# Performance work log

Hardware: AMD Instinct MI355X
Metric: run time of the kernel (lower is better)

Reference implementation:

```python
import jax, jax.numpy as jnp
import numpy as np

N, E, F, H, C = 100000, 1600000, 32, 64, 10


def setup_inputs() -> dict:
    key = jax.random.key(0)
    ks = jax.random.split(key, 12)
    x = jax.random.normal(ks[0], (N, F), dtype=jnp.float32)
    edge_index = jax.random.randint(ks[1], (2, E), 0, N, dtype=jnp.int64)
    edge_attr = jax.random.uniform(ks[2], (E,), dtype=jnp.float32)
    s = lambda k, shp, fan: jax.random.normal(k, shp, dtype=jnp.float32) / np.sqrt(fan)
    return {
        "x": x,
        "edge_index": edge_index,
        "edge_attr": edge_attr,
        "W1_rel": s(ks[3], (H, F), F),
        "b1_rel": jnp.zeros((H,), jnp.float32),
        "W1_root": s(ks[4], (H, F), F),
        "W2_rel": s(ks[5], (H, H), H),
        "b2_rel": jnp.zeros((H,), jnp.float32),
        "W2_root": s(ks[6], (H, H), H),
        "fc_w": s(ks[7], (C, H), H),
        "fc_b": jnp.zeros((C,), jnp.float32),
    }


def graph_conv(x, src, dst, ew, W_rel, b_rel, W_root):
    # message: x_j * e_ji, scatter-add at destination nodes (PyG GraphConv, aggr='add')
    msg = x[src] * ew[:, None]            # [E, d] gather + scale
    agg = jax.ops.segment_sum(msg, dst, num_segments=N)  # [N, d]
    return agg @ W_rel.T + b_rel + x @ W_root.T


def reference(x, edge_index, edge_attr, W1_rel, b1_rel, W1_root, W2_rel, b2_rel, W2_root, fc_w, fc_b):
    src, dst = edge_index[0], edge_index[1]
    h = jax.nn.relu(graph_conv(x, src, dst, edge_attr, W1_rel, b1_rel, W1_root))
    h = jax.nn.relu(graph_conv(h, src, dst, edge_attr, W2_rel, b2_rel, W2_root))
    return h @ fc_w.T + fc_b
```

## Files before the change

### kernel.cpp

```cpp
#include <hip/hip_runtime.h>

#define N_NODES 100000
#define EDGES   1600000
#define SCAN_NB ((N_NODES + 511) / 512)
#define GRID_HEAVY 2048

__device__ __forceinline__ unsigned pack_bf16(float a, float b) {
    unsigned ua = (__float_as_uint(a) + 0x8000u) >> 16;
    unsigned ub = (__float_as_uint(b) + 0x8000u) & 0xffff0000u;
    return ub | ua;
}
__device__ __forceinline__ float bflo(unsigned p) { return __uint_as_float(p << 16); }
__device__ __forceinline__ float bfhi(unsigned p) { return __uint_as_float(p & 0xffff0000u); }
__device__ __forceinline__ float bf2f(unsigned short u) { return __uint_as_float(((unsigned)u) << 16); }
__device__ __forceinline__ unsigned short f2bf(float x) { return (unsigned short)((__float_as_uint(x) + 0x8000u) >> 16); }

#define WAVE_FENCE() asm volatile("s_waitcnt lgkmcnt(0)" ::: "memory")

__global__ __launch_bounds__(256) void prep_kernel(
    const float* __restrict__ x, const int* __restrict__ ei,
    unsigned short* __restrict__ xb, int* __restrict__ cnt)
{
    int t = blockIdx.x * 256 + threadIdx.x;
    if (t < N_NODES * 32) xb[t] = f2bf(x[t]);
    if (t < EDGES) atomicAdd(&cnt[ei[EDGES + t]], 1);
}

__global__ __launch_bounds__(512) void scan1_kernel(
    const int* __restrict__ cnt, int* __restrict__ part, int* __restrict__ bsum)
{
    __shared__ int s[512];
    int tid = threadIdx.x;
    int gid = blockIdx.x * 512 + tid;
    int v = (gid < N_NODES) ? cnt[gid] : 0;
    s[tid] = v;
    __syncthreads();
    for (int off = 1; off < 512; off <<= 1) {
        int t = (tid >= off) ? s[tid - off] : 0;
        __syncthreads();
        s[tid] += t;
        __syncthreads();
    }
    if (gid < N_NODES) part[gid] = s[tid] - v;
    if (tid == 511) bsum[blockIdx.x] = s[511];
}

__global__ __launch_bounds__(256) void scan2_kernel(
    const int* __restrict__ bsum, int* __restrict__ bsumx)
{
    __shared__ int s[256];
    int tid = threadIdx.x;
    int v = (tid < SCAN_NB) ? bsum[tid] : 0;
    s[tid] = v;
    __syncthreads();
    for (int off = 1; off < 256; off <<= 1) {
        int t = (tid >= off) ? s[tid - off] : 0;
        __syncthreads();
        s[tid] += t;
        __syncthreads();
    }
    bsumx[tid] = s[tid] - v;
}

__global__ __launch_bounds__(512) void scan3_kernel(
    const int* __restrict__ part, const int* __restrict__ bsumx,
    int* __restrict__ offs, int* __restrict__ cursor)
{
    int gid = blockIdx.x * 512 + threadIdx.x;
    if (gid < N_NODES) {
        int o = part[gid] + bsumx[blockIdx.x];
        offs[gid] = o;
        cursor[gid] = o;
    }
    if (gid == 0) offs[N_NODES] = EDGES;
}

__global__ __launch_bounds__(256) void fill_kernel(
    const int* __restrict__ ei, const float* __restrict__ ew,
    int* __restrict__ cursor, uint2* __restrict__ bucket)
{
    int e = blockIdx.x * 256 + threadIdx.x;
    if (e >= EDGES) return;
    int d = ei[EDGES + e];
    int pos = atomicAdd(&cursor[d], 1);
    uint2 slot;
    slot.x = (unsigned)ei[e];
    slot.y = __float_as_uint(ew[e]);
    bucket[pos] = slot;
}

__global__ __launch_bounds__(256, 6) void agg_dense1_kernel(
    const float* __restrict__ x, const unsigned short* __restrict__ xb,
    const uint2* __restrict__ bucket, const int* __restrict__ offs,
    const float* __restrict__ W_rel, const float* __restrict__ b_rel,
    const float* __restrict__ W_root, unsigned short* __restrict__ h1b)
{
    __shared__ unsigned pkrel[16][64];
    __shared__ unsigned pkroot[16][64];
    __shared__ float sb[64];
    __shared__ __align__(16) float accr[4][32];
    __shared__ __align__(16) float xr[4][32];
    int tid = threadIdx.x;
    for (int i = tid; i < 16 * 64; i += 256) {
        int k = i >> 6, h = i & 63;
        pkrel[k][h]  = pack_bf16(W_rel[h * 32 + 2 * k],  W_rel[h * 32 + 2 * k + 1]);
        pkroot[k][h] = pack_bf16(W_root[h * 32 + 2 * k], W_root[h * 32 + 2 * k + 1]);
    }
    if (tid < 64) sb[tid] = b_rel[tid];
    __syncthreads();

    int w = tid >> 6, lane = tid & 63;
    int sub = lane >> 5, f = lane & 31;
    int wid = blockIdx.x * 4 + w;

    for (int node = wid; node < N_NODES; node += GRID_HEAVY * 4) {
        float acc = 0.f;
        if (sub == 0) xr[w][f] = x[(size_t)node * 32 + f];
        int o0 = __builtin_amdgcn_readfirstlane(offs[node]);
        int o1 = __builtin_amdgcn_readfirstlane(offs[node + 1]);
        int j = o0;
        for (; j + 8 <= o1; j += 8) {
            uint2 b0 = bucket[j + 0 + sub], b1 = bucket[j + 2 + sub];
            uint2 b2 = bucket[j + 4 + sub], b3 = bucket[j + 6 + sub];
            float v0 = bf2f(xb[(size_t)b0.x * 32 + f]);
            float v1 = bf2f(xb[(size_t)b1.x * 32 + f]);
            float v2 = bf2f(xb[(size_t)b2.x * 32 + f]);
            float v3 = bf2f(xb[(size_t)b3.x * 32 + f]);
            acc += v0 * __uint_as_float(b0.y) + v1 * __uint_as_float(b1.y)
                 + v2 * __uint_as_float(b2.y) + v3 * __uint_as_float(b3.y);
        }
        for (; j + 2 <= o1; j += 2) {
            uint2 b = bucket[j + sub];
            acc += bf2f(xb[(size_t)b.x * 32 + f]) * __uint_as_float(b.y);
        }
        if (j + sub < o1) {
            uint2 b = bucket[j + sub];
            acc += bf2f(xb[(size_t)b.x * 32 + f]) * __uint_as_float(b.y);
        }
        acc += __shfl_xor(acc, 32);
        if (sub == 0) accr[w][f] = acc;
        WAVE_FENCE();
        {
            const float2* ap = (const float2*)accr[w];
            const float2* xp = (const float2*)xr[w];
            float sum = sb[lane];
            #pragma unroll
            for (int k = 0; k < 16; ++k) {
                float2 a = ap[k], xv = xp[k];
                unsigned pr = pkrel[k][lane], po = pkroot[k][lane];
                sum += a.x * bflo(pr) + a.y * bfhi(pr)
                     + xv.x * bflo(po) + xv.y * bfhi(po);
            }
            h1b[(size_t)node * 64 + lane] = f2bf(fmaxf(sum, 0.f));
        }
        WAVE_FENCE();
    }
}

__global__ __launch_bounds__(256, 6) void agg_dense2_kernel(
    const unsigned short* __restrict__ h1b, const uint2* __restrict__ bucket,
    const int* __restrict__ offs,
    const float* __restrict__ W_rel, const float* __restrict__ b_rel,
    const float* __restrict__ W_root,
    const float* __restrict__ fc_w, const float* __restrict__ fc_b,
    float* __restrict__ out)
{
    __shared__ unsigned pkrel[32][64];
    __shared__ unsigned pkroot[32][64];
    __shared__ unsigned pkfc[32][10];
    __shared__ float sb[64], sfb[10];
    __shared__ __align__(16) float accr[4][64];
    __shared__ __align__(16) float hvr[4][64];
    __shared__ __align__(16) float sh2r[4][64];
    int tid = threadIdx.x;
    for (int i = tid; i < 32 * 64; i += 256) {
        int k = i >> 6, h = i & 63;
        pkrel[k][h]  = pack_bf16(W_rel[h * 64 + 2 * k],  W_rel[h * 64 + 2 * k + 1]);
        pkroot[k][h] = pack_bf16(W_root[h * 64 + 2 * k], W_root[h * 64 + 2 * k + 1]);
    }
    for (int i = tid; i < 32 * 10; i += 256) {
        int k = i % 32, c = i / 32;
        pkfc[k][c] = pack_bf16(fc_w[c * 64 + 2 * k], fc_w[c * 64 + 2 * k + 1]);
    }
    if (tid < 64) sb[tid] = b_rel[tid];
    if (tid < 10) sfb[tid] = fc_b[tid];
    __syncthreads();

    int w = tid >> 6, lane = tid & 63;
    int wid = blockIdx.x * 4 + w;

    for (int node = wid; node < N_NODES; node += GRID_HEAVY * 4) {
        float acc = 0.f;
        float hv = bf2f(h1b[(size_t)node * 64 + lane]);
        int o0 = __builtin_amdgcn_readfirstlane(offs[node]);
        int o1 = __builtin_amdgcn_readfirstlane(offs[node + 1]);
        int j = o0;
        for (; j + 8 <= o1; j += 8) {
            uint2 s0 = bucket[j + 0], s1 = bucket[j + 1];
            uint2 s2 = bucket[j + 2], s3 = bucket[j + 3];
            uint2 s4 = bucket[j + 4], s5 = bucket[j + 5];
            uint2 s6 = bucket[j + 6], s7 = bucket[j + 7];
            float v0 = bf2f(h1b[(size_t)s0.x * 64 + lane]);
            float v1 = bf2f(h1b[(size_t)s1.x * 64 + lane]);
            float v2 = bf2f(h1b[(size_t)s2.x * 64 + lane]);
            float v3 = bf2f(h1b[(size_t)s3.x * 64 + lane]);
            float v4 = bf2f(h1b[(size_t)s4.x * 64 + lane]);
            float v5 = bf2f(h1b[(size_t)s5.x * 64 + lane]);
            float v6 = bf2f(h1b[(size_t)s6.x * 64 + lane]);
            float v7 = bf2f(h1b[(size_t)s7.x * 64 + lane]);
            acc += v0 * __uint_as_float(s0.y) + v1 * __uint_as_float(s1.y)
                 + v2 * __uint_as_float(s2.y) + v3 * __uint_as_float(s3.y)
                 + v4 * __uint_as_float(s4.y) + v5 * __uint_as_float(s5.y)
                 + v6 * __uint_as_float(s6.y) + v7 * __uint_as_float(s7.y);
        }
        for (; j + 4 <= o1; j += 4) {
            uint2 s0 = bucket[j + 0], s1 = bucket[j + 1];
            uint2 s2 = bucket[j + 2], s3 = bucket[j + 3];
            float v0 = bf2f(h1b[(size_t)s0.x * 64 + lane]);
            float v1 = bf2f(h1b[(size_t)s1.x * 64 + lane]);
            float v2 = bf2f(h1b[(size_t)s2.x * 64 + lane]);
            float v3 = bf2f(h1b[(size_t)s3.x * 64 + lane]);
            acc += v0 * __uint_as_float(s0.y) + v1 * __uint_as_float(s1.y)
                 + v2 * __uint_as_float(s2.y) + v3 * __uint_as_float(s3.y);
        }
        for (; j < o1; ++j) {
            uint2 s = bucket[j];
            acc += bf2f(h1b[(size_t)s.x * 64 + lane]) * __uint_as_float(s.y);
        }
        accr[w][lane] = acc;
        hvr[w][lane] = hv;
        WAVE_FENCE();
        {
            const float2* ap = (const float2*)accr[w];
            const float2* hp = (const float2*)hvr[w];
            float sum = sb[lane];
            #pragma unroll
            for (int k = 0; k < 32; ++k) {
                float2 a = ap[k], h2 = hp[k];
                unsigned pr = pkrel[k][lane], po = pkroot[k][lane];
                sum += a.x * bflo(pr) + a.y * bfhi(pr)
                     + h2.x * bflo(po) + h2.y * bfhi(po);
            }
            sh2r[w][lane] = fmaxf(sum, 0.f);
        }
        WAVE_FENCE();
        if (lane < 10) {
            const float2* sp = (const float2*)sh2r[w];
            float o = sfb[lane];
            #pragma unroll
            for (int k = 0; k < 32; ++k) {
                float2 s2 = sp[k];
                unsigned pc = pkfc[k][lane];
                o += s2.x * bflo(pc) + s2.y * bfhi(pc);
            }
            out[(size_t)node * 10 + lane] = o;
        }
        WAVE_FENCE();
    }
}

extern "C" void kernel_launch(void* const* d_in, const int* in_sizes, int n_in,
                              void* d_out, int out_size, void* d_ws, size_t ws_size,
                              hipStream_t stream) {
    const float* x       = (const float*)d_in[0];
    const int*   ei      = (const int*)d_in[1];
    const float* ew      = (const float*)d_in[2];
    const float* W1_rel  = (const float*)d_in[3];
    const float* b1_rel  = (const float*)d_in[4];
    const float* W1_root = (const float*)d_in[5];
    const float* W2_rel  = (const float*)d_in[6];
    const float* b2_rel  = (const float*)d_in[7];
    const float* W2_root = (const float*)d_in[8];
    const float* fc_w    = (const float*)d_in[9];
    const float* fc_b    = (const float*)d_in[10];
    float* out = (float*)d_out;

    uint2* bucket       = (uint2*)d_ws;
    unsigned short* h1b = (unsigned short*)(bucket + EDGES);
    unsigned short* xb  = h1b + (size_t)N_NODES * 64;
    int*   cnt    = (int*)(xb + (size_t)N_NODES * 32);
    int*   part   = cnt + N_NODES;
    int*   offs   = part + N_NODES;
    int*   cursor = offs + N_NODES + 1;
    int*   bsum   = cursor + N_NODES;
    int*   bsumx  = bsum + 256;

    hipMemsetAsync(cnt, 0, (size_t)N_NODES * sizeof(int), stream);

    prep_kernel<<<(N_NODES * 32 + 255) / 256, 256, 0, stream>>>(x, ei, xb, cnt);
    scan1_kernel<<<SCAN_NB, 512, 0, stream>>>(cnt, part, bsum);
    scan2_kernel<<<1, 256, 0, stream>>>(bsum, bsumx);
    scan3_kernel<<<SCAN_NB, 512, 0, stream>>>(part, bsumx, offs, cursor);
    fill_kernel<<<(EDGES + 255) / 256, 256, 0, stream>>>(ei, ew, cursor, bucket);

    agg_dense1_kernel<<<GRID_HEAVY, 256, 0, stream>>>(
        x, xb, bucket, offs, W1_rel, b1_rel, W1_root, h1b);
    agg_dense2_kernel<<<GRID_HEAVY, 256, 0, stream>>>(
        h1b, bucket, offs, W2_rel, b2_rel, W2_root, fc_w, fc_b, out);
}
```

Measured before the change: 494.8 us.

## Vectorize bf16 gathers to 32-bit loads and store fp32 weights in LDS

```diff
diff --git a/kernel.cpp b/kernel.cpp
--- a/kernel.cpp
+++ b/kernel.cpp
@@ -3,16 +3,9 @@
 #define N_NODES 100000
 #define EDGES   1600000
 #define SCAN_NB ((N_NODES + 511) / 512)
-#define GRID_HEAVY 2048
-
-__device__ __forceinline__ unsigned pack_bf16(float a, float b) {
-    unsigned ua = (__float_as_uint(a) + 0x8000u) >> 16;
-    unsigned ub = (__float_as_uint(b) + 0x8000u) & 0xffff0000u;
-    return ub | ua;
-}
+
 __device__ __forceinline__ float bflo(unsigned p) { return __uint_as_float(p << 16); }
 __device__ __forceinline__ float bfhi(unsigned p) { return __uint_as_float(p & 0xffff0000u); }
-__device__ __forceinline__ float bf2f(unsigned short u) { return __uint_as_float(((unsigned)u) << 16); }
 __device__ __forceinline__ unsigned short f2bf(float x) { return (unsigned short)((__float_as_uint(x) + 0x8000u) >> 16); }
 
 #define WAVE_FENCE() asm volatile("s_waitcnt lgkmcnt(0)" ::: "memory")
@@ -84,72 +77,82 @@
     int d = ei[EDGES + e];
     int pos = atomicAdd(&cursor[d], 1);
     uint2 slot;
-    slot.x = (unsigned)ei[e];
+    slot.x = ((unsigned)ei[e]) << 6;
     slot.y = __float_as_uint(ew[e]);
     bucket[pos] = slot;
 }
 
-__global__ __launch_bounds__(256, 6) void agg_dense1_kernel(
+__global__ __launch_bounds__(256, 8) void agg_dense1_kernel(
     const float* __restrict__ x, const unsigned short* __restrict__ xb,
     const uint2* __restrict__ bucket, const int* __restrict__ offs,
     const float* __restrict__ W_rel, const float* __restrict__ b_rel,
     const float* __restrict__ W_root, unsigned short* __restrict__ h1b)
 {
-    __shared__ unsigned pkrel[16][64];
-    __shared__ unsigned pkroot[16][64];
+    __shared__ float wrel1[32][64];
+    __shared__ float wroot1[32][64];
     __shared__ float sb[64];
     __shared__ __align__(16) float accr[4][32];
     __shared__ __align__(16) float xr[4][32];
     int tid = threadIdx.x;
-    for (int i = tid; i < 16 * 64; i += 256) {
+    for (int i = tid; i < 32 * 64; i += 256) {
         int k = i >> 6, h = i & 63;
-        pkrel[k][h]  = pack_bf16(W_rel[h * 32 + 2 * k],  W_rel[h * 32 + 2 * k + 1]);
-        pkroot[k][h] = pack_bf16(W_root[h * 32 + 2 * k], W_root[h * 32 + 2 * k + 1]);
+        wrel1[k][h]  = W_rel[h * 32 + k];
+        wroot1[k][h] = W_root[h * 32 + k];
     }
     if (tid < 64) sb[tid] = b_rel[tid];
     __syncthreads();
 
+    const char* xcb = (const char*)xb;
     int w = tid >> 6, lane = tid & 63;
-    int sub = lane >> 5, f = lane & 31;
+    int qsub = lane >> 4, f2 = lane & 15;
+    int voff = f2 << 2;
     int wid = blockIdx.x * 4 + w;
 
-    for (int node = wid; node < N_NODES; node += GRID_HEAVY * 4) {
-        float acc = 0.f;
-        if (sub == 0) xr[w][f] = x[(size_t)node * 32 + f];
+    for (int node = wid; node < N_NODES; node += gridDim.x * 4) {
+        float acc0 = 0.f, acc1 = 0.f;
+        if (lane < 32) xr[w][lane] = x[(size_t)node * 32 + lane];
         int o0 = __builtin_amdgcn_readfirstlane(offs[node]);
         int o1 = __builtin_amdgcn_readfirstlane(offs[node + 1]);
         int j = o0;
-        for (; j + 8 <= o1; j += 8) {
-            uint2 b0 = bucket[j + 0 + sub], b1 = bucket[j + 2 + sub];
-            uint2 b2 = bucket[j + 4 + sub], b3 = bucket[j + 6 + sub];
-            float v0 = bf2f(xb[(size_t)b0.x * 32 + f]);
-            float v1 = bf2f(xb[(size_t)b1.x * 32 + f]);
-            float v2 = bf2f(xb[(size_t)b2.x * 32 + f]);
-            float v3 = bf2f(xb[(size_t)b3.x * 32 + f]);
-            acc += v0 * __uint_as_float(b0.y) + v1 * __uint_as_float(b1.y)
-                 + v2 * __uint_as_float(b2.y) + v3 * __uint_as_float(b3.y);
-        }
-        for (; j + 2 <= o1; j += 2) {
-            uint2 b = bucket[j + sub];
-            acc += bf2f(xb[(size_t)b.x * 32 + f]) * __uint_as_float(b.y);
-        }
-        if (j + sub < o1) {
-            uint2 b = bucket[j + sub];
-            acc += bf2f(xb[(size_t)b.x * 32 + f]) * __uint_as_float(b.y);
-        }
-        acc += __shfl_xor(acc, 32);
-        if (sub == 0) accr[w][f] = acc;
+        for (; j + 16 <= o1; j += 16) {
+            uint2 b0 = bucket[j + 0  + qsub];
+            uint2 b1 = bucket[j + 4  + qsub];
+            uint2 b2 = bucket[j + 8  + qsub];
+            uint2 b3 = bucket[j + 12 + qsub];
+            unsigned p0 = *(const unsigned*)(xcb + (b0.x + voff));
+            unsigned p1 = *(const unsigned*)(xcb + (b1.x + voff));
+            unsigned p2 = *(const unsigned*)(xcb + (b2.x + voff));
+            unsigned p3 = *(const unsigned*)(xcb + (b3.x + voff));
+            float w0 = __uint_as_float(b0.y), w1 = __uint_as_float(b1.y);
+            float w2 = __uint_as_float(b2.y), w3 = __uint_as_float(b3.y);
+            acc0 += bflo(p0) * w0 + bflo(p1) * w1 + bflo(p2) * w2 + bflo(p3) * w3;
+            acc1 += bfhi(p0) * w0 + bfhi(p1) * w1 + bfhi(p2) * w2 + bfhi(p3) * w3;
+        }
+        for (; j < o1; j += 4) {
+            int jj = j + qsub;
+            uint2 b = bucket[jj < o1 ? jj : (o1 - 1)];
+            float wt = (jj < o1) ? __uint_as_float(b.y) : 0.f;
+            unsigned p = *(const unsigned*)(xcb + (b.x + voff));
+            acc0 += bflo(p) * wt;
+            acc1 += bfhi(p) * wt;
+        }
+        acc0 += __shfl_xor(acc0, 16); acc0 += __shfl_xor(acc0, 32);
+        acc1 += __shfl_xor(acc1, 16); acc1 += __shfl_xor(acc1, 32);
+        if (lane < 16) {
+            accr[w][2 * f2]     = acc0;
+            accr[w][2 * f2 + 1] = acc1;
+        }
         WAVE_FENCE();
         {
-            const float2* ap = (const float2*)accr[w];
-            const float2* xp = (const float2*)xr[w];
+            const float* ap = accr[w];
+            const float* xp = xr[w];
             float sum = sb[lane];
             #pragma unroll
-            for (int k = 0; k < 16; ++k) {
-                float2 a = ap[k], xv = xp[k];
-                unsigned pr = pkrel[k][lane], po = pkroot[k][lane];
-                sum += a.x * bflo(pr) + a.y * bfhi(pr)
-                     + xv.x * bflo(po) + xv.y * bfhi(po);
+            for (int k = 0; k < 32; k += 2) {
+                float2 a  = *(const float2*)&ap[k];
+                float2 xv = *(const float2*)&xp[k];
+                sum += a.x  * wrel1[k][lane]  + a.y  * wrel1[k + 1][lane]
+                     + xv.x * wroot1[k][lane] + xv.y * wroot1[k + 1][lane];
             }
             h1b[(size_t)node * 64 + lane] = f2bf(fmaxf(sum, 0.f));
         }
@@ -157,7 +160,7 @@
     }
 }
 
-__global__ __launch_bounds__(256, 6) void agg_dense2_kernel(
+__global__ __launch_bounds__(256, 4) void agg_dense2_kernel(
     const unsigned short* __restrict__ h1b, const uint2* __restrict__ bucket,
     const int* __restrict__ offs,
     const float* __restrict__ W_rel, const float* __restrict__ b_rel,
@@ -165,81 +168,96 @@
     const float* __restrict__ fc_w, const float* __restrict__ fc_b,
     float* __restrict__ out)
 {
-    __shared__ unsigned pkrel[32][64];
-    __shared__ unsigned pkroot[32][64];
+    __shared__ float wrel2[64][64];
+    __shared__ float wroot2[64][64];
     __shared__ unsigned pkfc[32][10];
     __shared__ float sb[64], sfb[10];
     __shared__ __align__(16) float accr[4][64];
     __shared__ __align__(16) float hvr[4][64];
     __shared__ __align__(16) float sh2r[4][64];
     int tid = threadIdx.x;
-    for (int i = tid; i < 32 * 64; i += 256) {
+    for (int i = tid; i < 64 * 64; i += 256) {
         int k = i >> 6, h = i & 63;
-        pkrel[k][h]  = pack_bf16(W_rel[h * 64 + 2 * k],  W_rel[h * 64 + 2 * k + 1]);
-        pkroot[k][h] = pack_bf16(W_root[h * 64 + 2 * k], W_root[h * 64 + 2 * k + 1]);
+        wrel2[k][h]  = W_rel[h * 64 + k];
+        wroot2[k][h] = W_root[h * 64 + k];
     }
     for (int i = tid; i < 32 * 10; i += 256) {
         int k = i % 32, c = i / 32;
-        pkfc[k][c] = pack_bf16(fc_w[c * 64 + 2 * k], fc_w[c * 64 + 2 * k + 1]);
+        unsigned lo = (__float_as_uint(fc_w[c * 64 + 2 * k]) + 0x8000u) >> 16;
+        unsigned hi = (__float_as_uint(fc_w[c * 64 + 2 * k + 1]) + 0x8000u) & 0xffff0000u;
+        pkfc[k][c] = hi | lo;
     }
     if (tid < 64) sb[tid] = b_rel[tid];
     if (tid < 10) sfb[tid] = fc_b[tid];
     __syncthreads();
 
+    const char* h1cb = (const char*)h1b;
     int w = tid >> 6, lane = tid & 63;
+    int sub = lane >> 5, f2 = lane & 31;
+    int voff = f2 << 2;
     int wid = blockIdx.x * 4 + w;
 
-    for (int node = wid; node < N_NODES; node += GRID_HEAVY * 4) {
-        float acc = 0.f;
-        float hv = bf2f(h1b[(size_t)node * 64 + lane]);
+    for (int node = wid; node < N_NODES; node += gridDim.x * 4) {
+        float acc0 = 0.f, acc1 = 0.f;
+        if (sub == 0) {
+            unsigned hp = *(const unsigned*)(h1cb + (((unsigned)node << 7) + voff));
+            hvr[w][2 * f2]     = bflo(hp);
+            hvr[w][2 * f2 + 1] = bfhi(hp);
+        }
         int o0 = __builtin_amdgcn_readfirstlane(offs[node]);
         int o1 = __builtin_amdgcn_readfirstlane(offs[node + 1]);
         int j = o0;
-        for (; j + 8 <= o1; j += 8) {
-            uint2 s0 = bucket[j + 0], s1 = bucket[j + 1];
-            uint2 s2 = bucket[j + 2], s3 = bucket[j + 3];
-            uint2 s4 = bucket[j + 4], s5 = bucket[j + 5];
-            uint2 s6 = bucket[j + 6], s7 = bucket[j + 7];
-            float v0 = bf2f(h1b[(size_t)s0.x * 64 + lane]);
-            float v1 = bf2f(h1b[(size_t)s1.x * 64 + lane]);
-            float v2 = bf2f(h1b[(size_t)s2.x * 64 + lane]);
-            float v3 = bf2f(h1b[(size_t)s3.x * 64 + lane]);
-            float v4 = bf2f(h1b[(size_t)s4.x * 64 + lane]);
-            float v5 = bf2f(h1b[(size_t)s5.x * 64 + lane]);
-            float v6 = bf2f(h1b[(size_t)s6.x * 64 + lane]);
-            float v7 = bf2f(h1b[(size_t)s7.x * 64 + lane]);
-            acc += v0 * __uint_as_float(s0.y) + v1 * __uint_as_float(s1.y)
-                 + v2 * __uint_as_float(s2.y) + v3 * __uint_as_float(s3.y)
-                 + v4 * __uint_as_float(s4.y) + v5 * __uint_as_float(s5.y)
-                 + v6 * __uint_as_float(s6.y) + v7 * __uint_as_float(s7.y);
-        }
-        for (; j + 4 <= o1; j += 4) {
-            uint2 s0 = bucket[j + 0], s1 = bucket[j + 1];
-            uint2 s2 = bucket[j + 2], s3 = bucket[j + 3];
-            float v0 = bf2f(h1b[(size_t)s0.x * 64 + lane]);
-            float v1 = bf2f(h1b[(size_t)s1.x * 64 + lane]);
-            float v2 = bf2f(h1b[(size_t)s2.x * 64 + lane]);
-            float v3 = bf2f(h1b[(size_t)s3.x * 64 + lane]);
-            acc += v0 * __uint_as_float(s0.y) + v1 * __uint_as_float(s1.y)
-                 + v2 * __uint_as_float(s2.y) + v3 * __uint_as_float(s3.y);
-        }
-        for (; j < o1; ++j) {
-            uint2 s = bucket[j];
-            acc += bf2f(h1b[(size_t)s.x * 64 + lane]) * __uint_as_float(s.y);
-        }
-        accr[w][lane] = acc;
-        hvr[w][lane] = hv;
+        for (; j + 16 <= o1; j += 16) {
+            uint2 b0 = bucket[j + 0  + sub];
+            uint2 b1 = bucket[j + 2  + sub];
+            uint2 b2 = bucket[j + 4  + sub];
+            uint2 b3 = bucket[j + 6  + sub];
+            uint2 b4 = bucket[j + 8  + sub];
+            uint2 b5 = bucket[j + 10 + sub];
+            uint2 b6 = bucket[j + 12 + sub];
+            uint2 b7 = bucket[j + 14 + sub];
+            unsigned p0 = *(const unsigned*)(h1cb + ((b0.x << 1) + voff));
+            unsigned p1 = *(const unsigned*)(h1cb + ((b1.x << 1) + voff));
+            unsigned p2 = *(const unsigned*)(h1cb + ((b2.x << 1) + voff));
+            unsigned p3 = *(const unsigned*)(h1cb + ((b3.x << 1) + voff));
+            unsigned p4 = *(const unsigned*)(h1cb + ((b4.x << 1) + voff));
+            unsigned p5 = *(const unsigned*)(h1cb + ((b5.x << 1) + voff));
+            unsigned p6 = *(const unsigned*)(h1cb + ((b6.x << 1) + voff));
+            unsigned p7 = *(const unsigned*)(h1cb + ((b7.x << 1) + voff));
+            float w0 = __uint_as_float(b0.y), w1 = __uint_as_float(b1.y);
+            float w2 = __uint_as_float(b2.y), w3 = __uint_as_float(b3.y);
+            float w4 = __uint_as_float(b4.y), w5 = __uint_as_float(b5.y);
+            float w6 = __uint_as_float(b6.y), w7 = __uint_as_float(b7.y);
+            acc0 += bflo(p0) * w0 + bflo(p1) * w1 + bflo(p2) * w2 + bflo(p3) * w3
+                  + bflo(p4) * w4 + bflo(p5) * w5 + bflo(p6) * w6 + bflo(p7) * w7;
+            acc1 += bfhi(p0) * w0 + bfhi(p1) * w1 + bfhi(p2) * w2 + bfhi(p3) * w3
+                  + bfhi(p4) * w4 + bfhi(p5) * w5 + bfhi(p6) * w6 + bfhi(p7) * w7;
+        }
+        for (; j < o1; j += 2) {
+            int jj = j + sub;
+            uint2 b = bucket[jj < o1 ? jj : (o1 - 1)];
+            float wt = (jj < o1) ? __uint_as_float(b.y) : 0.f;
+            unsigned p = *(const unsigned*)(h1cb + ((b.x << 1) + voff));
+            acc0 += bflo(p) * wt;
+            acc1 += bfhi(p) * wt;
+        }
+        acc0 += __shfl_xor(acc0, 32);
+        acc1 += __shfl_xor(acc1, 32);
+        if (sub == 0) {
+            accr[w][2 * f2]     = acc0;
+            accr[w][2 * f2 + 1] = acc1;
+        }
         WAVE_FENCE();
         {
-            const float2* ap = (const float2*)accr[w];
-            const float2* hp = (const float2*)hvr[w];
+            const float* ap = accr[w];
+            const float* hp = hvr[w];
             float sum = sb[lane];
             #pragma unroll
-            for (int k = 0; k < 32; ++k) {
-                float2 a = ap[k], h2 = hp[k];
-                unsigned pr = pkrel[k][lane], po = pkroot[k][lane];
-                sum += a.x * bflo(pr) + a.y * bfhi(pr)
-                     + h2.x * bflo(po) + h2.y * bfhi(po);
+            for (int k = 0; k < 64; k += 2) {
+                float2 a  = *(const float2*)&ap[k];
+                float2 h2 = *(const float2*)&hp[k];
+                sum += a.x  * wrel2[k][lane]  + a.y  * wrel2[k + 1][lane]
+                     + h2.x * wroot2[k][lane] + h2.y * wroot2[k + 1][lane];
             }
             sh2r[w][lane] = fmaxf(sum, 0.f);
         }
@@ -293,8 +311,8 @@
     scan3_kernel<<<SCAN_NB, 512, 0, stream>>>(part, bsumx, offs, cursor);
     fill_kernel<<<(EDGES + 255) / 256, 256, 0, stream>>>(ei, ew, cursor, bucket);
 
-    agg_dense1_kernel<<<GRID_HEAVY, 256, 0, stream>>>(
+    agg_dense1_kernel<<<2048, 256, 0, stream>>>(
         x, xb, bucket, offs, W1_rel, b1_rel, W1_root, h1b);
-    agg_dense2_kernel<<<GRID_HEAVY, 256, 0, stream>>>(
+    agg_dense2_kernel<<<1024, 256, 0, stream>>>(
         h1b, bucket, offs, W2_rel, b2_rel, W2_root, fc_w, fc_b, out);
 }
```

New measurement: 497.6 us. About the same (+0.6%).
